# Kernel tuning notes

Hardware: AMD Instinct MI355X
Metric: run time of the kernel (lower is better)

Reference implementation:

```python
import jax, jax.numpy as jnp
import numpy as np

N = 50000
E = 800000
F_IN = 64
F_OUT = 64


def setup_inputs() -> dict:
    key = jax.random.key(0)
    ks = jax.random.split(key, 14)
    x = jax.random.normal(ks[0], (N, F_IN), dtype=jnp.float32)
    row_low = jax.random.randint(ks[1], (E,), 0, N)
    col_low = jax.random.randint(ks[2], (E,), 0, N)
    val_low = jax.random.uniform(ks[3], (E,), dtype=jnp.float32)
    row_high = jax.random.randint(ks[4], (E,), 0, N)
    col_high = jax.random.randint(ks[5], (E,), 0, N)
    val_high = jax.random.uniform(ks[6], (E,), dtype=jnp.float32)
    # xavier-uniform style init for weights
    def xavier(k, shape):
        fan_in, fan_out = shape[0], shape[1]
        bound = float(np.sqrt(6.0 / (fan_in + fan_out)))
        return jax.random.uniform(k, shape, jnp.float32, -bound, bound)
    W_low = xavier(ks[7], (F_IN, F_OUT))
    W_high = xavier(ks[8], (F_IN, F_OUT))
    W_mlp = xavier(ks[9], (F_IN, F_OUT))
    a_low = xavier(ks[10], (F_OUT, 1))
    a_high = xavier(ks[11], (F_OUT, 1))
    a_mlp = xavier(ks[12], (F_OUT, 1))
    att3 = xavier(ks[13], (3, 3))
    return dict(x=x, row_low=row_low, col_low=col_low, val_low=val_low,
                row_high=row_high, col_high=col_high, val_high=val_high,
                W_low=W_low, W_high=W_high, W_mlp=W_mlp,
                a_low=a_low, a_high=a_high, a_mlp=a_mlp, att3=att3)


def _spmm(row, col, val, h, n):
    # (sparse adj) @ h : gather source rows, scale by edge weight, scatter-add to dest
    return jax.ops.segment_sum(val[:, None] * h[col], row, num_segments=n)


def reference(x, row_low, col_low, val_low, row_high, col_high, val_high,
              W_low, W_high, W_mlp, a_low, a_high, a_mlp, att3):
    n = x.shape[0]
    out_low = jax.nn.relu(_spmm(row_low, col_low, val_low, x @ W_low, n))
    out_high = jax.nn.relu(_spmm(row_high, col_high, val_high, x @ W_high, n))
    out_mlp = jax.nn.relu(x @ W_mlp)
    T = 3.0
    feats = jnp.concatenate([out_low @ a_low, out_high @ a_high, out_mlp @ a_mlp], axis=1)  # [N,3]
    logits = (jax.nn.sigmoid(feats) @ att3) / T
    att = jax.nn.softmax(logits, axis=1)  # [N,3]
    return 3.0 * (att[:, 0:1] * out_low + att[:, 1:2] * out_high + att[:, 2:3] * out_mlp)
```

## Files before the change

kernel.cpp:

```cpp
#include <hip/hip_runtime.h>
#include <hip/hip_fp16.h>


#define NNODE 50000
#define NEDGE 800000
#define NBUCK 391
#define CAP   2880
#define SORT_BLOCKS (2 * NBUCK)
#define GEMM_BLOCKS ((NNODE + 63) / 64)

typedef __attribute__((ext_vector_type(8))) short short8v;
typedef __attribute__((ext_vector_type(4))) float float4v;

__device__ __forceinline__ unsigned short f2bf(float f) {
    unsigned u = __float_as_uint(f);
    u += 0x7FFFu + ((u >> 16) & 1u);
    return (unsigned short)(u >> 16);
}
__device__ __forceinline__ __half2 u_as_h2(unsigned u) {
    return *reinterpret_cast<__half2*>(&u);
}

__global__ __launch_bounds__(256)
void zero_kernel(unsigned int* __restrict__ g)
{
    const int i = blockIdx.x * 256 + threadIdx.x;
    if (i < 2 * NBUCK) g[i] = 0u;
}

__global__ __launch_bounds__(512)
void scatter_kernel(const int* __restrict__ row_low, const int* __restrict__ col_low,
                    const float* __restrict__ val_low,
                    const int* __restrict__ row_high, const int* __restrict__ col_high,
                    const float* __restrict__ val_high,
                    unsigned int* __restrict__ gcursor, uint2* __restrict__ packed)
{
    __shared__ unsigned int hist_s[2 * NBUCK];
    __shared__ unsigned int base_s[2 * NBUCK];
    const int t = threadIdx.x;
    const int ebase = blockIdx.x * 8192;

    for (int i = t; i < 2 * NBUCK; i += 512) hist_s[i] = 0u;
    __syncthreads();

    int rows[16]; unsigned int rank[16];
#pragma unroll
    for (int j = 0; j < 16; ++j) {
        const int e = ebase + j * 512 + t;
        rows[j] = 0; rank[j] = 0u;
        if (e < 2 * NEDGE) {
            const int r = (e < NEDGE) ? row_low[e] : row_high[e - NEDGE];
            const int fb = ((e < NEDGE) ? 0 : NBUCK) + (r >> 7);
            rows[j] = r;
            rank[j] = atomicAdd(&hist_s[fb], 1u);
        }
    }
    __syncthreads();
    for (int i = t; i < 2 * NBUCK; i += 512) {
        const unsigned int c = hist_s[i];
        base_s[i] = c ? atomicAdd(&gcursor[i], c) : 0u;
    }
    __syncthreads();
#pragma unroll
    for (int j = 0; j < 16; ++j) {
        const int e = ebase + j * 512 + t;
        if (e < 2 * NEDGE) {
            const int g = (e >= NEDGE);
            const int ee = e - g * NEDGE;
            const int r = rows[j];
            const int c = g ? col_high[ee] : col_low[ee];
            const float v = g ? val_high[ee] : val_low[ee];
            const int fb = g * NBUCK + (r >> 7);
            const unsigned int pos = base_s[fb] + rank[j];
            if (pos < CAP) {
                uint2 pk;
                pk.x = (unsigned int)c | ((unsigned int)(r & 127) << 16);
                pk.y = (unsigned)__half_as_ushort(__float2half(v));
                packed[(size_t)fb * CAP + pos] = pk;
            }
        }
    }
}

__global__ __launch_bounds__(256)
void sort_gemm_kernel(const uint2* __restrict__ packed,
                      unsigned int* __restrict__ rec4,
                      const unsigned int* __restrict__ gcursor,
                      int* __restrict__ rs, int* __restrict__ rc,
                      const float* __restrict__ x,
                      const float* __restrict__ Wl, const float* __restrict__ Wh,
                      const float* __restrict__ Wm,
                      unsigned short* __restrict__ hl16,
                      unsigned short* __restrict__ hh16,
                      unsigned short* __restrict__ hm16)
{
    __shared__ char smem[27648];
    const int t = threadIdx.x;

    if (blockIdx.x < SORT_BLOCKS) {
        unsigned int*  rec_s = (unsigned int*)smem;
        unsigned char* row_s = (unsigned char*)(rec_s + CAP);
        unsigned int*  hist  = (unsigned int*)(row_s + CAP);
        unsigned int*  offs  = hist + 128;
        unsigned int*  cur   = offs + 128;
        unsigned int*  wsum2 = cur + 128;

        const int fb = blockIdx.x;
        const uint2* __restrict__ seg = packed + (size_t)fb * CAP;
        unsigned int* __restrict__ rout = rec4 + (size_t)fb * CAP;
        int cnt = (int)gcursor[fb];
        if (cnt > CAP) cnt = CAP;

        if (t < 128) { hist[t] = 0u; cur[t] = 0u; }
        __syncthreads();

        for (int i = t; i < cnt; i += 256) {
            const uint2 p = seg[i];
            const unsigned r = (p.x >> 16) & 127u;
            rec_s[i] = (p.x & 0xFFFFu) | (p.y << 16);
            row_s[i] = (unsigned char)r;
            atomicAdd(&hist[r], 1u);
        }
        __syncthreads();

        unsigned pv = 0, xinc = 0;
        if (t < 128) {
            pv = (hist[t] + 7u) & ~7u;
            xinc = pv;
#pragma unroll
            for (int d = 1; d < 64; d <<= 1) {
                unsigned y = __shfl_up(xinc, d, 64);
                if ((t & 63) >= d) xinc += y;
            }
            if ((t & 63) == 63) wsum2[t >> 6] = xinc;
        }
        __syncthreads();
        if (t < 128) {
            const unsigned add = (t >= 64) ? wsum2[0] : 0u;
            offs[t] = add + xinc - pv;
        }
        __syncthreads();

        for (int i = t; i < cnt; i += 256) {
            const unsigned r = row_s[i];
            const unsigned pos = offs[r] + atomicAdd(&cur[r], 1u);
            if (pos < CAP) rout[pos] = rec_s[i];
        }
        if (t < 128) {
            const unsigned b = offs[t] + hist[t];
            const unsigned e = offs[t] + ((hist[t] + 7u) & ~7u);
            for (unsigned u = b; u < e && u < CAP; ++u) rout[u] = 0u;
        }

        if (t < 128) {
            const int g = (fb >= NBUCK);
            const int node = ((fb - g * NBUCK) << 7) + t;
            if (node < NNODE) {
                const unsigned P = (hist[t] + 7u) & ~7u;
                const int avail = CAP - (int)offs[t];
                int nq = (int)(P >> 2);
                int nqa = avail > 0 ? ((avail >> 2) & ~1) : 0;
                if (nq > nqa) nq = nqa;
                rs[g * NNODE + node] = fb * CAP + (int)offs[t];
                rc[g * NNODE + node] = nq;
            }
        }
    } else {
        typedef unsigned short wt_t[64][72];
        wt_t* wt = (wt_t*)smem;

#pragma unroll 1
        for (int m = 0; m < 3; ++m) {
            const float* __restrict__ W = (m == 0) ? Wl : (m == 1) ? Wh : Wm;
            for (int i = t; i < 4096; i += 256) {
                const int k = i >> 6, c = i & 63;
                wt[m][c][k] = f2bf(W[i]);
            }
        }
        __syncthreads();

        const int wid = t >> 6, lane = t & 63;
        const int node0 = (blockIdx.x - SORT_BLOCKS) * 64 + wid * 16;
        if (node0 >= NNODE) return;
        const int arow = lane & 15;
        const int hi = lane >> 4;

        const float* __restrict__ xr = x + (size_t)(node0 + arow) * 64 + hi * 8;
        const float4 pa0 = *(const float4*)(xr + 0);
        const float4 pa1 = *(const float4*)(xr + 4);
        const float4 pb0 = *(const float4*)(xr + 32);
        const float4 pb1 = *(const float4*)(xr + 36);
        short8v a0, a1;
        a0[0] = (short)f2bf(pa0.x); a0[1] = (short)f2bf(pa0.y);
        a0[2] = (short)f2bf(pa0.z); a0[3] = (short)f2bf(pa0.w);
        a0[4] = (short)f2bf(pa1.x); a0[5] = (short)f2bf(pa1.y);
        a0[6] = (short)f2bf(pa1.z); a0[7] = (short)f2bf(pa1.w);
        a1[0] = (short)f2bf(pb0.x); a1[1] = (short)f2bf(pb0.y);
        a1[2] = (short)f2bf(pb0.z); a1[3] = (short)f2bf(pb0.w);
        a1[4] = (short)f2bf(pb1.x); a1[5] = (short)f2bf(pb1.y);
        a1[6] = (short)f2bf(pb1.z); a1[7] = (short)f2bf(pb1.w);

#pragma unroll 1
        for (int m = 0; m < 3; ++m) {
            unsigned short* __restrict__ H = (m == 0) ? hl16 : (m == 1) ? hh16 : hm16;
            float4v acc0 = {0.f, 0.f, 0.f, 0.f}, acc1 = {0.f, 0.f, 0.f, 0.f};
            float4v acc2 = {0.f, 0.f, 0.f, 0.f}, acc3 = {0.f, 0.f, 0.f, 0.f};

#define DO_CT(CT, ACC)                                                          \
            {                                                                   \
                const short8v b0 = *(const short8v*)&wt[m][CT * 16 + arow][hi * 8]; \
                const short8v b1 = *(const short8v*)&wt[m][CT * 16 + arow][32 + hi * 8]; \
                ACC = __builtin_amdgcn_mfma_f32_16x16x32_bf16(a0, b0, ACC, 0, 0, 0); \
                ACC = __builtin_amdgcn_mfma_f32_16x16x32_bf16(a1, b1, ACC, 0, 0, 0); \
            }
            DO_CT(0, acc0) DO_CT(1, acc1) DO_CT(2, acc2) DO_CT(3, acc3)
#undef DO_CT

            const bool rl = (m == 2);
#define ST_CT(CT, ACC)                                                          \
            {                                                                   \
                _Pragma("unroll")                                               \
                for (int r = 0; r < 4; ++r) {                                   \
                    float v = ACC[r];                                           \
                    if (rl) v = fmaxf(v, 0.f);                                  \
                    H[(size_t)(node0 + hi * 4 + r) * 64 + CT * 16 + arow] =     \
                        __half_as_ushort(__float2half(v));                      \
                }                                                               \
            }
            ST_CT(0, acc0) ST_CT(1, acc1) ST_CT(2, acc2) ST_CT(3, acc3)
#undef ST_CT
        }
    }
}

__global__ __launch_bounds__(256, 8)
void spmm_finalize_kernel(const unsigned int* __restrict__ rec4,
                          const int* __restrict__ rs, const int* __restrict__ rc,
                          const unsigned short* __restrict__ hl16,
                          const unsigned short* __restrict__ hh16,
                          const unsigned short* __restrict__ hm16,
                          const float* __restrict__ aL, const float* __restrict__ aH,
                          const float* __restrict__ aM, const float* __restrict__ att3,
                          float* __restrict__ out)
{
    const int wid = threadIdx.x >> 6;
    const int lane = threadIdx.x & 63;
    const int sub = lane >> 4;
    const int f4 = (lane & 15) << 2;
    const unsigned fb2 = (unsigned)(f4 * 2);
    const int node = blockIdx.x * 4 + wid;
    if (node >= NNODE) return;

    const int sL = __builtin_amdgcn_readfirstlane(rs[node]);
    const int nqL = __builtin_amdgcn_readfirstlane(rc[node]);
    const int sH = __builtin_amdgcn_readfirstlane(rs[NNODE + node]);
    const int nqH = __builtin_amdgcn_readfirstlane(rc[NNODE + node]);
    const unsigned int* __restrict__ segL = rec4 + sL + sub;
    const unsigned int* __restrict__ segH = rec4 + sH + sub;
    const int nqm = (nqL > nqH) ? nqL : nqH;

    const __half2 hz2 = u_as_h2(0u);
    __half2 aL0a = hz2, aL1a = hz2, aL0b = hz2, aL1b = hz2;
    __half2 aH0a = hz2, aH1a = hz2, aH0b = hz2, aH1b = hz2;

#pragma unroll 1
    for (int q = 0; q < nqm; q += 2) {
        const unsigned rL0 = segL[q * 4];
        const unsigned rL1 = segL[q * 4 + 4];
        const unsigned rH0 = segH[q * 4];
        const unsigned rH1 = segH[q * 4 + 4];
        const uint2 uL0 = *(const uint2*)((const char*)hl16 + (size_t)(((rL0 & 0xFFFFu) << 7) + fb2));
        const uint2 uL1 = *(const uint2*)((const char*)hl16 + (size_t)(((rL1 & 0xFFFFu) << 7) + fb2));
        const uint2 uH0 = *(const uint2*)((const char*)hh16 + (size_t)(((rH0 & 0xFFFFu) << 7) + fb2));
        const uint2 uH1 = *(const uint2*)((const char*)hh16 + (size_t)(((rH1 & 0xFFFFu) << 7) + fb2));
        __builtin_amdgcn_sched_barrier(0);
        const unsigned dL0 = (rL0 & 0xFFFF0000u) | (rL0 >> 16);
        const unsigned dL1 = (rL1 & 0xFFFF0000u) | (rL1 >> 16);
        const unsigned dH0 = (rH0 & 0xFFFF0000u) | (rH0 >> 16);
        const unsigned dH1 = (rH1 & 0xFFFF0000u) | (rH1 >> 16);
        const __half2 vL0 = u_as_h2((q     < nqL) ? dL0 : 0u);
        const __half2 vL1 = u_as_h2((q + 1 < nqL) ? dL1 : 0u);
        const __half2 vH0 = u_as_h2((q     < nqH) ? dH0 : 0u);
        const __half2 vH1 = u_as_h2((q + 1 < nqH) ? dH1 : 0u);
        aL0a = __hfma2(u_as_h2(uL0.x), vL0, aL0a);
        aL1a = __hfma2(u_as_h2(uL0.y), vL0, aL1a);
        aL0b = __hfma2(u_as_h2(uL1.x), vL1, aL0b);
        aL1b = __hfma2(u_as_h2(uL1.y), vL1, aL1b);
        aH0a = __hfma2(u_as_h2(uH0.x), vH0, aH0a);
        aH1a = __hfma2(u_as_h2(uH0.y), vH0, aH1a);
        aH0b = __hfma2(u_as_h2(uH1.x), vH1, aH0b);
        aH1b = __hfma2(u_as_h2(uH1.y), vH1, aH1b);
    }

    float lx = __low2float(aL0a) + __low2float(aL0b);
    float ly = __high2float(aL0a) + __high2float(aL0b);
    float lz = __low2float(aL1a) + __low2float(aL1b);
    float lw = __high2float(aL1a) + __high2float(aL1b);
    float hx = __low2float(aH0a) + __low2float(aH0b);
    float hy = __high2float(aH0a) + __high2float(aH0b);
    float hz = __low2float(aH1a) + __low2float(aH1b);
    float hw = __high2float(aH1a) + __high2float(aH1b);

    lx += __shfl_xor(lx, 16, 64); ly += __shfl_xor(ly, 16, 64);
    lz += __shfl_xor(lz, 16, 64); lw += __shfl_xor(lw, 16, 64);
    hx += __shfl_xor(hx, 16, 64); hy += __shfl_xor(hy, 16, 64);
    hz += __shfl_xor(hz, 16, 64); hw += __shfl_xor(hw, 16, 64);
    lx += __shfl_xor(lx, 32, 64); ly += __shfl_xor(ly, 32, 64);
    lz += __shfl_xor(lz, 32, 64); lw += __shfl_xor(lw, 32, 64);
    hx += __shfl_xor(hx, 32, 64); hy += __shfl_xor(hy, 32, 64);
    hz += __shfl_xor(hz, 32, 64); hw += __shfl_xor(hw, 32, 64);

    const float olx = fmaxf(lx, 0.f), oly = fmaxf(ly, 0.f);
    const float olz = fmaxf(lz, 0.f), olw = fmaxf(lw, 0.f);
    const float ohx = fmaxf(hx, 0.f), ohy = fmaxf(hy, 0.f);
    const float ohz = fmaxf(hz, 0.f), ohw = fmaxf(hw, 0.f);

    const uint2 om2 = *(const uint2*)&hm16[(size_t)node * 64 + f4];
    const float omx = __low2float(u_as_h2(om2.x));
    const float omy = __high2float(u_as_h2(om2.x));
    const float omz = __low2float(u_as_h2(om2.y));
    const float omw = __high2float(u_as_h2(om2.y));

    const float4 aL4 = *(const float4*)&aL[f4];
    const float4 aH4 = *(const float4*)&aH[f4];
    const float4 aM4 = *(const float4*)&aM[f4];

    float f0 = olx * aL4.x + oly * aL4.y + olz * aL4.z + olw * aL4.w;
    float f1 = ohx * aH4.x + ohy * aH4.y + ohz * aH4.z + ohw * aH4.w;
    float f2 = omx * aM4.x + omy * aM4.y + omz * aM4.z + omw * aM4.w;
#pragma unroll
    for (int msk = 1; msk < 16; msk <<= 1) {
        f0 += __shfl_xor(f0, msk, 64);
        f1 += __shfl_xor(f1, msk, 64);
        f2 += __shfl_xor(f2, msk, 64);
    }
    const float s0 = 1.f / (1.f + __expf(-f0));
    const float s1 = 1.f / (1.f + __expf(-f1));
    const float s2 = 1.f / (1.f + __expf(-f2));
    const float invT = 1.f / 3.f;
    const float l0g = (s0 * att3[0] + s1 * att3[3] + s2 * att3[6]) * invT;
    const float l1g = (s0 * att3[1] + s1 * att3[4] + s2 * att3[7]) * invT;
    const float l2g = (s0 * att3[2] + s1 * att3[5] + s2 * att3[8]) * invT;
    const float mx = fmaxf(l0g, fmaxf(l1g, l2g));
    const float e0 = __expf(l0g - mx);
    const float e1 = __expf(l1g - mx);
    const float e2 = __expf(l2g - mx);
    const float inv = 1.f / (e0 + e1 + e2);
    const float wl = 3.f * inv * e0, wh = 3.f * inv * e1, wm = 3.f * inv * e2;

    if (lane < 16) {
        float4 o;
        o.x = wl * olx + wh * ohx + wm * omx;
        o.y = wl * oly + wh * ohy + wm * omy;
        o.z = wl * olz + wh * ohz + wm * omz;
        o.w = wl * olw + wh * ohw + wm * omw;
        *(float4*)&out[(size_t)node * 64 + f4] = o;
    }
}

extern "C" void kernel_launch(void* const* d_in, const int* in_sizes, int n_in,
                              void* d_out, int out_size, void* d_ws, size_t ws_size,
                              hipStream_t stream)
{
    const float* x        = (const float*)d_in[0];
    const int*   row_low  = (const int*)  d_in[1];
    const int*   col_low  = (const int*)  d_in[2];
    const float* val_low  = (const float*)d_in[3];
    const int*   row_high = (const int*)  d_in[4];
    const int*   col_high = (const int*)  d_in[5];
    const float* val_high = (const float*)d_in[6];
    const float* W_low    = (const float*)d_in[7];
    const float* W_high   = (const float*)d_in[8];
    const float* W_mlp    = (const float*)d_in[9];
    const float* a_low    = (const float*)d_in[10];
    const float* a_high   = (const float*)d_in[11];
    const float* a_mlp    = (const float*)d_in[12];
    const float* att3     = (const float*)d_in[13];
    float* out = (float*)d_out;

    const size_t NM = (size_t)NNODE * 64;
    const size_t NSLOT = (size_t)2 * NBUCK * CAP;

    unsigned short* hl16    = (unsigned short*)d_ws;
    unsigned short* hh16    = hl16 + NM;
    unsigned short* hm16    = hh16 + NM;
    uint2*          packed  = (uint2*)(hm16 + NM);
    unsigned int*   rec4    = (unsigned int*)(packed + NSLOT);
    unsigned int*   gcursor = rec4 + NSLOT;
    int*            rs      = (int*)(gcursor + 2 * NBUCK);
    int*            rc      = rs + 2 * NNODE;

    zero_kernel<<<(2 * NBUCK + 255) / 256, 256, 0, stream>>>(gcursor);

    scatter_kernel<<<(2 * NEDGE + 8191) / 8192, 512, 0, stream>>>(
        row_low, col_low, val_low, row_high, col_high, val_high, gcursor, packed);

    sort_gemm_kernel<<<SORT_BLOCKS + GEMM_BLOCKS, 256, 0, stream>>>(
        packed, rec4, gcursor, rs, rc,
        x, W_low, W_high, W_mlp, hl16, hh16, hm16);

    spmm_finalize_kernel<<<(NNODE + 3) / 4, 256, 0, stream>>>(
        rec4, rs, rc, hl16, hh16, hm16, a_low, a_high, a_mlp, att3, out);
}
```

Baseline: 85.59 us.

## Use 256-row buckets, larger scatter blocks, and 4-way unrolled gather loop

Halves the number of row buckets (256 rows each, larger capacity per bucket) so the sort phase uses all 256 threads, with a 4-wave prefix scan. The scatter kernel handles twice as many edges per block, which means fewer blocks and fewer global cursor atomics. The SpMM gather loop is unrolled to 4 edges per iteration to keep more loads in flight, and the launch bound is relaxed to 4 waves per SIMD so the extra registers fit. The trade-offs are fewer scatter and sort blocks, which means less parallelism, and possible occupancy loss in the SpMM kernel.

New measurement: 91.00 us. 1.06x slower.

```diff
diff --git a/kernel.cpp b/kernel.cpp
--- a/kernel.cpp
+++ b/kernel.cpp
@@ -4,8 +4,8 @@
 
 #define NNODE 50000
 #define NEDGE 800000
-#define NBUCK 391
-#define CAP   2880
+#define NBUCK 196
+#define CAP   5504
 #define SORT_BLOCKS (2 * NBUCK)
 #define GEMM_BLOCKS ((NNODE + 63) / 64)
 
@@ -38,19 +38,19 @@
     __shared__ unsigned int hist_s[2 * NBUCK];
     __shared__ unsigned int base_s[2 * NBUCK];
     const int t = threadIdx.x;
-    const int ebase = blockIdx.x * 8192;
+    const int ebase = blockIdx.x * 16384;
 
     for (int i = t; i < 2 * NBUCK; i += 512) hist_s[i] = 0u;
     __syncthreads();
 
-    int rows[16]; unsigned int rank[16];
+    int rows[32]; unsigned int rank[32];
 #pragma unroll
-    for (int j = 0; j < 16; ++j) {
+    for (int j = 0; j < 32; ++j) {
         const int e = ebase + j * 512 + t;
         rows[j] = 0; rank[j] = 0u;
         if (e < 2 * NEDGE) {
             const int r = (e < NEDGE) ? row_low[e] : row_high[e - NEDGE];
-            const int fb = ((e < NEDGE) ? 0 : NBUCK) + (r >> 7);
+            const int fb = ((e < NEDGE) ? 0 : NBUCK) + (r >> 8);
             rows[j] = r;
             rank[j] = atomicAdd(&hist_s[fb], 1u);
         }
@@ -62,7 +62,7 @@
     }
     __syncthreads();
 #pragma unroll
-    for (int j = 0; j < 16; ++j) {
+    for (int j = 0; j < 32; ++j) {
         const int e = ebase + j * 512 + t;
         if (e < 2 * NEDGE) {
             const int g = (e >= NEDGE);
@@ -70,11 +70,11 @@
             const int r = rows[j];
             const int c = g ? col_high[ee] : col_low[ee];
             const float v = g ? val_high[ee] : val_low[ee];
-            const int fb = g * NBUCK + (r >> 7);
+            const int fb = g * NBUCK + (r >> 8);
             const unsigned int pos = base_s[fb] + rank[j];
             if (pos < CAP) {
                 uint2 pk;
-                pk.x = (unsigned int)c | ((unsigned int)(r & 127) << 16);
+                pk.x = (unsigned int)c | ((unsigned int)(r & 255) << 16);
                 pk.y = (unsigned)__half_as_ushort(__float2half(v));
                 packed[(size_t)fb * CAP + pos] = pk;
             }
@@ -94,16 +94,16 @@
                       unsigned short* __restrict__ hh16,
                       unsigned short* __restrict__ hm16)
 {
-    __shared__ char smem[27648];
+    __shared__ char smem[30720];
     const int t = threadIdx.x;
 
     if (blockIdx.x < SORT_BLOCKS) {
-        unsigned int*  rec_s = (unsigned int*)smem;
-        unsigned char* row_s = (unsigned char*)(rec_s + CAP);
-        unsigned int*  hist  = (unsigned int*)(row_s + CAP);
-        unsigned int*  offs  = hist + 128;
-        unsigned int*  cur   = offs + 128;
-        unsigned int*  wsum2 = cur + 128;
+        unsigned int*   rec_s = (unsigned int*)smem;
+        unsigned char*  row_s = (unsigned char*)(rec_s + CAP);
+        unsigned int*   hist  = (unsigned int*)(row_s + CAP);
+        unsigned int*   offs  = hist + 256;
+        unsigned int*   cur   = offs + 256;
+        unsigned int*   wsum4 = cur + 256;
 
         const int fb = blockIdx.x;
         const uint2* __restrict__ seg = packed + (size_t)fb * CAP;
@@ -111,32 +111,33 @@
         int cnt = (int)gcursor[fb];
         if (cnt > CAP) cnt = CAP;
 
-        if (t < 128) { hist[t] = 0u; cur[t] = 0u; }
+        hist[t] = 0u; cur[t] = 0u;
         __syncthreads();
 
         for (int i = t; i < cnt; i += 256) {
             const uint2 p = seg[i];
-            const unsigned r = (p.x >> 16) & 127u;
+            const unsigned r = (p.x >> 16) & 255u;
             rec_s[i] = (p.x & 0xFFFFu) | (p.y << 16);
             row_s[i] = (unsigned char)r;
             atomicAdd(&hist[r], 1u);
         }
         __syncthreads();
 
-        unsigned pv = 0, xinc = 0;
-        if (t < 128) {
-            pv = (hist[t] + 7u) & ~7u;
-            xinc = pv;
+        const unsigned pv = (hist[t] + 7u) & ~7u;
+        unsigned xinc = pv;
 #pragma unroll
-            for (int d = 1; d < 64; d <<= 1) {
-                unsigned y = __shfl_up(xinc, d, 64);
-                if ((t & 63) >= d) xinc += y;
-            }
-            if ((t & 63) == 63) wsum2[t >> 6] = xinc;
-        }
+        for (int d = 1; d < 64; d <<= 1) {
+            unsigned y = __shfl_up(xinc, d, 64);
+            if ((t & 63) >= d) xinc += y;
+        }
+        if ((t & 63) == 63) wsum4[t >> 6] = xinc;
         __syncthreads();
-        if (t < 128) {
-            const unsigned add = (t >= 64) ? wsum2[0] : 0u;
+        {
+            const int w = t >> 6;
+            unsigned add = 0;
+            if (w > 0) add += wsum4[0];
+            if (w > 1) add += wsum4[1];
+            if (w > 2) add += wsum4[2];
             offs[t] = add + xinc - pv;
         }
         __syncthreads();
@@ -146,15 +147,15 @@
             const unsigned pos = offs[r] + atomicAdd(&cur[r], 1u);
             if (pos < CAP) rout[pos] = rec_s[i];
         }
-        if (t < 128) {
+        {
             const unsigned b = offs[t] + hist[t];
             const unsigned e = offs[t] + ((hist[t] + 7u) & ~7u);
             for (unsigned u = b; u < e && u < CAP; ++u) rout[u] = 0u;
         }
 
-        if (t < 128) {
+        {
             const int g = (fb >= NBUCK);
-            const int node = ((fb - g * NBUCK) << 7) + t;
+            const int node = ((fb - g * NBUCK) << 8) + t;
             if (node < NNODE) {
                 const unsigned P = (hist[t] + 7u) & ~7u;
                 const int avail = CAP - (int)offs[t];
@@ -233,7 +234,10 @@
     }
 }
 
-__global__ __launch_bounds__(256, 8)
+#define GATH(hg_, rr_) (*(const uint2*)((const char*)(hg_) + (size_t)((((rr_) & 0xFFFFu) << 7) + fb2)))
+#define DSWAP(rr_) (((rr_) & 0xFFFF0000u) | ((rr_) >> 16))
+
+__global__ __launch_bounds__(256, 4)
 void spmm_finalize_kernel(const unsigned int* __restrict__ rec4,
                           const int* __restrict__ rs, const int* __restrict__ rc,
                           const unsigned short* __restrict__ hl16,
@@ -263,25 +267,54 @@
     __half2 aL0a = hz2, aL1a = hz2, aL0b = hz2, aL1b = hz2;
     __half2 aH0a = hz2, aH1a = hz2, aH0b = hz2, aH1b = hz2;
 
+    int q = 0;
 #pragma unroll 1
-    for (int q = 0; q < nqm; q += 2) {
-        const unsigned rL0 = segL[q * 4];
-        const unsigned rL1 = segL[q * 4 + 4];
-        const unsigned rH0 = segH[q * 4];
-        const unsigned rH1 = segH[q * 4 + 4];
-        const uint2 uL0 = *(const uint2*)((const char*)hl16 + (size_t)(((rL0 & 0xFFFFu) << 7) + fb2));
-        const uint2 uL1 = *(const uint2*)((const char*)hl16 + (size_t)(((rL1 & 0xFFFFu) << 7) + fb2));
-        const uint2 uH0 = *(const uint2*)((const char*)hh16 + (size_t)(((rH0 & 0xFFFFu) << 7) + fb2));
-        const uint2 uH1 = *(const uint2*)((const char*)hh16 + (size_t)(((rH1 & 0xFFFFu) << 7) + fb2));
+    for (; q + 4 <= nqm; q += 4) {
+        const unsigned rL0 = segL[q * 4],      rL1 = segL[q * 4 + 4];
+        const unsigned rL2 = segL[q * 4 + 8],  rL3 = segL[q * 4 + 12];
+        const unsigned rH0 = segH[q * 4],      rH1 = segH[q * 4 + 4];
+        const unsigned rH2 = segH[q * 4 + 8],  rH3 = segH[q * 4 + 12];
+        const uint2 uL0 = GATH(hl16, rL0), uL1 = GATH(hl16, rL1);
+        const uint2 uL2 = GATH(hl16, rL2), uL3 = GATH(hl16, rL3);
+        const uint2 uH0 = GATH(hh16, rH0), uH1 = GATH(hh16, rH1);
+        const uint2 uH2 = GATH(hh16, rH2), uH3 = GATH(hh16, rH3);
         __builtin_amdgcn_sched_barrier(0);
-        const unsigned dL0 = (rL0 & 0xFFFF0000u) | (rL0 >> 16);
-        const unsigned dL1 = (rL1 & 0xFFFF0000u) | (rL1 >> 16);
-        const unsigned dH0 = (rH0 & 0xFFFF0000u) | (rH0 >> 16);
-        const unsigned dH1 = (rH1 & 0xFFFF0000u) | (rH1 >> 16);
-        const __half2 vL0 = u_as_h2((q     < nqL) ? dL0 : 0u);
-        const __half2 vL1 = u_as_h2((q + 1 < nqL) ? dL1 : 0u);
-        const __half2 vH0 = u_as_h2((q     < nqH) ? dH0 : 0u);
-        const __half2 vH1 = u_as_h2((q + 1 < nqH) ? dH1 : 0u);
+        const __half2 vL0 = u_as_h2((q     < nqL) ? DSWAP(rL0) : 0u);
+        const __half2 vL1 = u_as_h2((q + 1 < nqL) ? DSWAP(rL1) : 0u);
+        const __half2 vL2 = u_as_h2((q + 2 < nqL) ? DSWAP(rL2) : 0u);
+        const __half2 vL3 = u_as_h2((q + 3 < nqL) ? DSWAP(rL3) : 0u);
+        const __half2 vH0 = u_as_h2((q     < nqH) ? DSWAP(rH0) : 0u);
+        const __half2 vH1 = u_as_h2((q + 1 < nqH) ? DSWAP(rH1) : 0u);
+        const __half2 vH2 = u_as_h2((q + 2 < nqH) ? DSWAP(rH2) : 0u);
+        const __half2 vH3 = u_as_h2((q + 3 < nqH) ? DSWAP(rH3) : 0u);
+        aL0a = __hfma2(u_as_h2(uL0.x), vL0, aL0a);
+        aL1a = __hfma2(u_as_h2(uL0.y), vL0, aL1a);
+        aL0b = __hfma2(u_as_h2(uL1.x), vL1, aL0b);
+        aL1b = __hfma2(u_as_h2(uL1.y), vL1, aL1b);
+        aL0a = __hfma2(u_as_h2(uL2.x), vL2, aL0a);
+        aL1a = __hfma2(u_as_h2(uL2.y), vL2, aL1a);
+        aL0b = __hfma2(u_as_h2(uL3.x), vL3, aL0b);
+        aL1b = __hfma2(u_as_h2(uL3.y), vL3, aL1b);
+        aH0a = __hfma2(u_as_h2(uH0.x), vH0, aH0a);
+        aH1a = __hfma2(u_as_h2(uH0.y), vH0, aH1a);
+        aH0b = __hfma2(u_as_h2(uH1.x), vH1, aH0b);
+        aH1b = __hfma2(u_as_h2(uH1.y), vH1, aH1b);
+        aH0a = __hfma2(u_as_h2(uH2.x), vH2, aH0a);
+        aH1a = __hfma2(u_as_h2(uH2.y), vH2, aH1a);
+        aH0b = __hfma2(u_as_h2(uH3.x), vH3, aH0b);
+        aH1b = __hfma2(u_as_h2(uH3.y), vH3, aH1b);
+    }
+#pragma unroll 1
+    for (; q + 2 <= nqm; q += 2) {
+        const unsigned rL0 = segL[q * 4], rL1 = segL[q * 4 + 4];
+        const unsigned rH0 = segH[q * 4], rH1 = segH[q * 4 + 4];
+        const uint2 uL0 = GATH(hl16, rL0), uL1 = GATH(hl16, rL1);
+        const uint2 uH0 = GATH(hh16, rH0), uH1 = GATH(hh16, rH1);
+        __builtin_amdgcn_sched_barrier(0);
+        const __half2 vL0 = u_as_h2((q     < nqL) ? DSWAP(rL0) : 0u);
+        const __half2 vL1 = u_as_h2((q + 1 < nqL) ? DSWAP(rL1) : 0u);
+        const __half2 vH0 = u_as_h2((q     < nqH) ? DSWAP(rH0) : 0u);
+        const __half2 vH1 = u_as_h2((q + 1 < nqH) ? DSWAP(rH1) : 0u);
         aL0a = __hfma2(u_as_h2(uL0.x), vL0, aL0a);
         aL1a = __hfma2(u_as_h2(uL0.y), vL0, aL1a);
         aL0b = __hfma2(u_as_h2(uL1.x), vL1, aL0b);
@@ -392,7 +425,7 @@
 
     zero_kernel<<<(2 * NBUCK + 255) / 256, 256, 0, stream>>>(gcursor);
 
-    scatter_kernel<<<(2 * NEDGE + 8191) / 8192, 512, 0, stream>>>(
+    scatter_kernel<<<(2 * NEDGE + 16383) / 16384, 512, 0, stream>>>(
         row_low, col_low, val_low, row_high, col_high, val_high, gcursor, packed);
 
     sort_gemm_kernel<<<SORT_BLOCKS + GEMM_BLOCKS, 256, 0, stream>>>(
```
